# Kernel tuning notes

Hardware: AMD Instinct MI355X
Metric: run time of the kernel (lower is better)

Reference implementation:

```python
import jax, jax.numpy as jnp
import numpy as np

B, N, M = 4096, 512, 64
SEQ_W = 8
HID, CTRL_OUT = 256, 128
SHIFT_VEC = (-1, 0, 1)
L = len(SHIFT_VEC)
PARAM_SIZE = M + 1 + 1 + L + 1  # k(M), beta, g, s(L), gamma
# circular-shift gather indices: idx[i, j] = (i + shift_vec[j]) mod N
IDX = np.mod(np.arange(N)[:, None] + np.array(SHIFT_VEC)[None, :], N)


def setup_inputs() -> dict:
    key = jax.random.key(0)
    ks = jax.random.split(key, 12)
    def w(k, shape, fan_in):
        return jax.random.normal(k, shape, jnp.float32) / np.sqrt(fan_in).astype(np.float32)
    in_size = SEQ_W + 1 + M  # controller input: x (seq_width+1) + prev_read (M)
    wr = jax.random.uniform(ks[3], (B, N), jnp.float32)
    wr = wr / wr.sum(axis=1, keepdims=True)
    ww = jax.random.uniform(ks[4], (B, N), jnp.float32)
    ww = ww / ww.sum(axis=1, keepdims=True)
    return {
        "x": jax.random.normal(ks[0], (B, SEQ_W + 1), jnp.float32),
        "prev_read": jax.random.normal(ks[1], (B, M), jnp.float32),
        "bank": jax.random.uniform(ks[2], (B, N, M), jnp.float32) * 0.1 + 1e-6,
        "w_read": wr,
        "w_write": ww,
        "ctrl_W0": w(ks[5], (in_size, HID), in_size), "ctrl_b0": jnp.zeros(HID, jnp.float32),
        "ctrl_W1": w(ks[6], (HID, HID), HID), "ctrl_b1": jnp.zeros(HID, jnp.float32),
        "ctrl_Wout": w(ks[7], (HID, CTRL_OUT), HID), "ctrl_bout": jnp.zeros(CTRL_OUT, jnp.float32),
        "repr_W": w(ks[8], (CTRL_OUT, 2 * PARAM_SIZE + 2 * M), CTRL_OUT),
        "repr_b": jnp.zeros(2 * PARAM_SIZE + 2 * M, jnp.float32),
        "out_W": w(ks[9], (CTRL_OUT + M, SEQ_W), CTRL_OUT + M),
        "out_b": jnp.zeros(SEQ_W, jnp.float32),
    }


def _split(v):
    # k [B,M], beta [B,1], g [B,1], s [B,L], gamma [B,1]
    return v[:, :M], v[:, M:M + 1], v[:, M + 1:M + 2], v[:, M + 2:M + 2 + L], v[:, -1:]


def _address(param, w_prev, bank):
    k, beta, g, s, gamma = param
    kt = jnp.tanh(k)
    # cosine similarity along M (torch CosineSimilarity, eps=1e-8)
    dot = jnp.einsum('bnm,bm->bn', bank, kt)
    denom = jnp.linalg.norm(bank, axis=2) * jnp.linalg.norm(kt, axis=1, keepdims=True)
    cos = dot / jnp.maximum(denom, 1e-8)
    wc = jax.nn.softmax(jax.nn.softplus(beta) * cos, axis=1)
    gg = jax.nn.sigmoid(g)
    wg = gg * wc + (1.0 - gg) * w_prev
    sm = jax.nn.softmax(s, axis=1)
    # vectorized circular shift: ws[b,i] = sum_j wg[b,(i+shift_j)%N] * sm[b,j]
    ws = jnp.einsum('bnl,bl->bn', wg[:, IDX], sm)
    gamma = jax.nn.softplus(gamma) + 1.0
    wsh = ws ** gamma
    return wsh / wsh.sum(axis=1, keepdims=True)


def reference(x, prev_read, bank, w_read, w_write,
              ctrl_W0, ctrl_b0, ctrl_W1, ctrl_b1, ctrl_Wout, ctrl_bout,
              repr_W, repr_b, out_W, out_b):
    ctrl_in = jnp.concatenate([x, prev_read], axis=1)
    h = jax.nn.leaky_relu(ctrl_in @ ctrl_W0 + ctrl_b0)
    h = jax.nn.leaky_relu(h @ ctrl_W1 + ctrl_b1)
    ctrl_out = jnp.tanh(h @ ctrl_Wout + ctrl_bout)
    reprx = ctrl_out @ repr_W + repr_b
    read_param = _split(reprx[:, :PARAM_SIZE])
    write_param = _split(reprx[:, PARAM_SIZE:2 * PARAM_SIZE])
    e = jax.nn.sigmoid(reprx[:, 2 * PARAM_SIZE:2 * PARAM_SIZE + M])
    a = jnp.tanh(reprx[:, 2 * PARAM_SIZE + M:])
    rw = _address(read_param, w_read, bank)
    read = jnp.einsum('bn,bnm->bm', rw, bank)  # memory read
    wwt = _address(write_param, w_write, bank)
    # erase then add: bank - w*e + w*a
    new_bank = bank + wwt[:, :, None] * (a - e)[:, None, :]
    seq_out = jax.nn.sigmoid(jnp.concatenate([ctrl_out, read], axis=1) @ out_W + out_b)
    return seq_out, new_bank
```

## Files before the change

kernel.cpp:

```cpp
#include <hip/hip_runtime.h>
#include <hip/hip_bf16.h>
#include <math.h>

#define B_TOT 4096
#define NN 512
#define MM 64
#define HID 256
#define COUT 128
#define PSZ 70
#define REPRN 268
#define IN_SZ 73
#define WS_STRIDE 352
#define BT 8


__device__ __forceinline__ float sigmoidf_(float v){ return 1.f/(1.f+expf(-v)); }
__device__ __forceinline__ float softplusf_(float v){ return v > 20.f ? v : log1pf(expf(v)); }
__device__ __forceinline__ float leakyf_(float v){ return v >= 0.f ? v : 0.01f*v; }

__device__ __forceinline__ float wave_sum(float v){
  #pragma unroll
  for (int o = 32; o; o >>= 1) v += __shfl_xor(v, o);
  return v;
}
__device__ __forceinline__ float wave_max(float v){
  #pragma unroll
  for (int o = 32; o; o >>= 1) v = fmaxf(v, __shfl_xor(v, o));
  return v;
}
__device__ float block_sum(float v, float* red){
  v = wave_sum(v);
  int w = threadIdx.x >> 6, l = threadIdx.x & 63;
  __syncthreads();
  if (l == 0) red[w] = v;
  __syncthreads();
  return red[0] + red[1] + red[2] + red[3];
}
__device__ float block_max(float v, float* red){
  v = wave_max(v);
  int w = threadIdx.x >> 6, l = threadIdx.x & 63;
  __syncthreads();
  if (l == 0) red[w] = v;
  __syncthreads();
  return fmaxf(fmaxf(red[0], red[1]), fmaxf(red[2], red[3]));
}

__global__ __launch_bounds__(256) void k_ctrl(
    const float* __restrict__ x, const float* __restrict__ prev_read,
    const float* __restrict__ W0, const float* __restrict__ b0,
    const float* __restrict__ W1, const float* __restrict__ b1,
    const float* __restrict__ Wout, const float* __restrict__ bout,
    const float* __restrict__ rW, const float* __restrict__ rb,
    float* __restrict__ pws)
{
  __shared__ float cin[BT][80];
  __shared__ float sA[BT][256];
  __shared__ float sB[BT][256];
  __shared__ float sR[BT][272];
  const int t = threadIdx.x;
  const int bbase = blockIdx.x * BT;

  for (int idx = t; idx < BT * IN_SZ; idx += 256){
    int bb = idx / IN_SZ, i = idx - bb * IN_SZ;
    int b = bbase + bb;
    cin[bb][i] = (i < 9) ? x[b * 9 + i] : prev_read[b * MM + (i - 9)];
  }
  __syncthreads();

  {
    float acc[BT];
    #pragma unroll
    for (int bb = 0; bb < BT; ++bb) acc[bb] = 0.f;
    for (int i = 0; i < IN_SZ; ++i){
      float w = W0[i * 256 + t];
      #pragma unroll
      for (int bb = 0; bb < BT; ++bb) acc[bb] += cin[bb][i] * w;
    }
    float bias = b0[t];
    #pragma unroll
    for (int bb = 0; bb < BT; ++bb) sA[bb][t] = leakyf_(acc[bb] + bias);
  }
  __syncthreads();

  {
    float acc[BT];
    #pragma unroll
    for (int bb = 0; bb < BT; ++bb) acc[bb] = 0.f;
    for (int i = 0; i < 256; ++i){
      float w = W1[i * 256 + t];
      #pragma unroll
      for (int bb = 0; bb < BT; ++bb) acc[bb] += sA[bb][i] * w;
    }
    float bias = b1[t];
    #pragma unroll
    for (int bb = 0; bb < BT; ++bb) sB[bb][t] = leakyf_(acc[bb] + bias);
  }
  __syncthreads();

  if (t < COUT){
    float acc[BT];
    #pragma unroll
    for (int bb = 0; bb < BT; ++bb) acc[bb] = 0.f;
    for (int i = 0; i < 256; ++i){
      float w = Wout[i * COUT + t];
      #pragma unroll
      for (int bb = 0; bb < BT; ++bb) acc[bb] += sB[bb][i] * w;
    }
    float bias = bout[t];
    #pragma unroll
    for (int bb = 0; bb < BT; ++bb){
      float v = tanhf(acc[bb] + bias);
      sA[bb][t] = v;
      pws[(size_t)(bbase + bb) * WS_STRIDE + t] = v;
    }
  }
  __syncthreads();

  {
    float acc1[BT], acc2[BT];
    #pragma unroll
    for (int bb = 0; bb < BT; ++bb){ acc1[bb] = 0.f; acc2[bb] = 0.f; }
    const bool has2 = (t + 256) < REPRN;
    for (int i = 0; i < COUT; ++i){
      float w1 = rW[i * REPRN + t];
      float w2 = has2 ? rW[i * REPRN + t + 256] : 0.f;
      #pragma unroll
      for (int bb = 0; bb < BT; ++bb){
        float c = sA[bb][i];
        acc1[bb] += c * w1;
        acc2[bb] += c * w2;
      }
    }
    float r1 = rb[t];
    float r2 = has2 ? rb[t + 256] : 0.f;
    #pragma unroll
    for (int bb = 0; bb < BT; ++bb){
      sR[bb][t] = acc1[bb] + r1;
      if (has2) sR[bb][t + 256] = acc2[bb] + r2;
    }
  }
  __syncthreads();

  for (int bb = 0; bb < BT; ++bb){
    float* pb = pws + (size_t)(bbase + bb) * WS_STRIDE;
    if (t < 64){
      float kt = tanhf(sR[bb][t]);
      pb[128 + t] = kt;
      float s = wave_sum(kt * kt);
      if (t == 0) pb[320] = sqrtf(s);
    } else if (t < 128){
      int m = t - 64;
      float kt = tanhf(sR[bb][PSZ + m]);
      pb[192 + m] = kt;
      float s = wave_sum(kt * kt);
      if (m == 0) pb[328] = sqrtf(s);
    } else if (t < 192){
      int m = t - 128;
      float e = sigmoidf_(sR[bb][2 * PSZ + m]);
      float a = tanhf(sR[bb][2 * PSZ + MM + m]);
      pb[256 + m] = a - e;
    } else if (t == 192 || t == 193){
      int off = (t == 192) ? 0 : PSZ;
      int po  = (t == 192) ? 320 : 328;
      float beta = sR[bb][off + 64];
      float g    = sR[bb][off + 65];
      float s0 = sR[bb][off + 66], s1 = sR[bb][off + 67], s2 = sR[bb][off + 68];
      float gm = sR[bb][off + 69];
      pb[po + 1] = softplusf_(beta);
      pb[po + 2] = sigmoidf_(g);
      float mx = fmaxf(s0, fmaxf(s1, s2));
      float e0 = expf(s0 - mx), e1 = expf(s1 - mx), e2 = expf(s2 - mx);
      float inv = 1.f / (e0 + e1 + e2);
      pb[po + 3] = e0 * inv; pb[po + 4] = e1 * inv; pb[po + 5] = e2 * inv;
      pb[po + 6] = softplusf_(gm) + 1.f;
    }
  }
}

__device__ void address_head(const float* __restrict__ dot, const float* __restrict__ ssv,
                             float knorm, float beta, float g,
                             float sm0, float sm1, float sm2, float gamma,
                             const float* __restrict__ wprev,
                             float* tmp, float* wfin, float* red)
{
  const int t = threadIdx.x;
  float c1 = dot[t]       / fmaxf(sqrtf(ssv[t])       * knorm, 1e-8f);
  float c2 = dot[t + 256] / fmaxf(sqrtf(ssv[t + 256]) * knorm, 1e-8f);
  float v1 = beta * c1, v2 = beta * c2;
  float vmax = block_max(fmaxf(v1, v2), red);
  float e1 = expf(v1 - vmax), e2 = expf(v2 - vmax);
  float S = block_sum(e1 + e2, red);
  float inv = 1.f / S;
  float wg1 = g * (e1 * inv) + (1.f - g) * wprev[t];
  float wg2 = g * (e2 * inv) + (1.f - g) * wprev[t + 256];
  tmp[t] = wg1; tmp[t + 256] = wg2;
  __syncthreads();
  float ws1 = tmp[(t + 511) & 511] * sm0 + wg1 * sm1 + tmp[(t + 1) & 511] * sm2;
  float ws2 = tmp[(t + 255) & 511] * sm0 + wg2 * sm1 + tmp[(t + 257) & 511] * sm2;
  float p1 = powf(ws1, gamma), p2 = powf(ws2, gamma);
  float S2 = block_sum(p1 + p2, red);
  float inv2 = 1.f / S2;
  wfin[t] = p1 * inv2; wfin[t + 256] = p2 * inv2;
  __syncthreads();
}

__global__ __launch_bounds__(256) void k_head(
    const float* __restrict__ bank,
    const float* __restrict__ w_read, const float* __restrict__ w_write,
    const float* __restrict__ outW, const float* __restrict__ outb,
    const float* __restrict__ pws,
    float* __restrict__ out)
{
  __shared__ float dotr[512], dotw[512], ssv[512], tmp[512], wfr[512], wfw[512];
  __shared__ float red[4];
  __shared__ float readpart[4][64];
  __shared__ float readv[64];

  const int b = blockIdx.x;
  const int t = threadIdx.x;
  const int lane = t & 63, wave = t >> 6;
  const int mg = lane & 15;
  const int rsub = lane >> 4;

  const float* bankB = bank + (size_t)b * (NN * MM);
  const float* pb = pws + (size_t)b * WS_STRIDE;

  const float4 ktr = *(const float4*)(pb + 128 + mg * 4);
  const float4 ktw = *(const float4*)(pb + 192 + mg * 4);

  for (int it = 0; it < 32; ++it){
    int n = it * 16 + wave * 4 + rsub;
    float4 p = *(const float4*)(bankB + n * MM + mg * 4);
    float dr = p.x * ktr.x + p.y * ktr.y + p.z * ktr.z + p.w * ktr.w;
    float dw = p.x * ktw.x + p.y * ktw.y + p.z * ktw.z + p.w * ktw.w;
    float sq = p.x * p.x + p.y * p.y + p.z * p.z + p.w * p.w;
    #pragma unroll
    for (int msk = 1; msk < 16; msk <<= 1){
      dr += __shfl_xor(dr, msk);
      dw += __shfl_xor(dw, msk);
      sq += __shfl_xor(sq, msk);
    }
    if (mg == 0){ dotr[n] = dr; dotw[n] = dw; ssv[n] = sq; }
  }
  __syncthreads();

  address_head(dotr, ssv, pb[320], pb[321], pb[322], pb[323], pb[324], pb[325], pb[326],
               w_read + (size_t)b * NN, tmp, wfr, red);
  address_head(dotw, ssv, pb[328], pb[329], pb[330], pb[331], pb[332], pb[333], pb[334],
               w_write + (size_t)b * NN, tmp, wfw, red);

  const float4 ae4 = *(const float4*)(pb + 256 + mg * 4);
  float* outBank = out + (size_t)B_TOT * 8 + (size_t)b * (NN * MM);
  float4 racc = make_float4(0.f, 0.f, 0.f, 0.f);
  for (int it = 0; it < 32; ++it){
    int n = it * 16 + wave * 4 + rsub;
    float4 p = *(const float4*)(bankB + n * MM + mg * 4);
    float wr = wfr[n], wwn = wfw[n];
    float4 q;
    q.x = p.x + wwn * ae4.x; q.y = p.y + wwn * ae4.y;
    q.z = p.z + wwn * ae4.z; q.w = p.w + wwn * ae4.w;
    *(float4*)(outBank + n * MM + mg * 4) = q;
    racc.x += wr * p.x; racc.y += wr * p.y; racc.z += wr * p.z; racc.w += wr * p.w;
  }
  racc.x += __shfl_xor(racc.x, 16); racc.x += __shfl_xor(racc.x, 32);
  racc.y += __shfl_xor(racc.y, 16); racc.y += __shfl_xor(racc.y, 32);
  racc.z += __shfl_xor(racc.z, 16); racc.z += __shfl_xor(racc.z, 32);
  racc.w += __shfl_xor(racc.w, 16); racc.w += __shfl_xor(racc.w, 32);
  if (lane < 16){
    readpart[wave][mg * 4 + 0] = racc.x;
    readpart[wave][mg * 4 + 1] = racc.y;
    readpart[wave][mg * 4 + 2] = racc.z;
    readpart[wave][mg * 4 + 3] = racc.w;
  }
  __syncthreads();
  if (t < 64) readv[t] = readpart[0][t] + readpart[1][t] + readpart[2][t] + readpart[3][t];
  __syncthreads();

  if (t < 8){
    float acc = outb[t];
    for (int i = 0; i < COUT; ++i) acc += pb[i] * outW[i * 8 + t];
    for (int m = 0; m < MM; ++m)   acc += readv[m] * outW[(COUT + m) * 8 + t];
    out[(size_t)b * 8 + t] = sigmoidf_(acc);
  }
}

extern "C" void kernel_launch(void* const* d_in, const int* in_sizes, int n_in,
                              void* d_out, int out_size, void* d_ws, size_t ws_size,
                              hipStream_t stream) {
  const float* x         = (const float*)d_in[0];
  const float* prev_read = (const float*)d_in[1];
  const float* bank      = (const float*)d_in[2];
  const float* w_read    = (const float*)d_in[3];
  const float* w_write   = (const float*)d_in[4];
  const float* W0        = (const float*)d_in[5];
  const float* b0        = (const float*)d_in[6];
  const float* W1        = (const float*)d_in[7];
  const float* b1        = (const float*)d_in[8];
  const float* Wout      = (const float*)d_in[9];
  const float* bout      = (const float*)d_in[10];
  const float* rW        = (const float*)d_in[11];
  const float* rb        = (const float*)d_in[12];
  const float* outW      = (const float*)d_in[13];
  const float* outb      = (const float*)d_in[14];
  float* out = (float*)d_out;
  float* pws = (float*)d_ws;

  k_ctrl<<<dim3(B_TOT / BT), dim3(256), 0, stream>>>(
      x, prev_read, W0, b0, W1, b1, Wout, bout, rW, rb, pws);
  k_head<<<dim3(B_TOT), dim3(256), 0, stream>>>(
      bank, w_read, w_write, outW, outb, pws, out);
}
```

Baseline: 1.067 ms.

## Cache each batch's bank slice in registers and widen head kernel to 512 threads

The head kernel now runs 512 threads per batch row and loads that row's bank slice once into registers (16 float4 per thread). The second pass, which writes the updated bank and accumulates the read vector, reuses those registers instead of reading the bank from global memory again, so bank reads are halved. The addressing and reductions are reworked for 8 waves, and the final output projection is spread over 64 threads with shuffle reductions. The cost is high register pressure (64 floats of bank per thread under launch_bounds(512,2)), which could spill or cut occupancy.

```diff
diff --git a/kernel.cpp b/kernel.cpp
--- a/kernel.cpp
+++ b/kernel.cpp
@@ -28,21 +28,28 @@
   for (int o = 32; o; o >>= 1) v = fmaxf(v, __shfl_xor(v, o));
   return v;
 }
-__device__ float block_sum(float v, float* red){
+
+__device__ float block_sum8(float v, float* red){
   v = wave_sum(v);
   int w = threadIdx.x >> 6, l = threadIdx.x & 63;
   __syncthreads();
   if (l == 0) red[w] = v;
   __syncthreads();
-  return red[0] + red[1] + red[2] + red[3];
-}
-__device__ float block_max(float v, float* red){
+  float s = 0.f;
+  #pragma unroll
+  for (int i = 0; i < 8; ++i) s += red[i];
+  return s;
+}
+__device__ float block_max8(float v, float* red){
   v = wave_max(v);
   int w = threadIdx.x >> 6, l = threadIdx.x & 63;
   __syncthreads();
   if (l == 0) red[w] = v;
   __syncthreads();
-  return fmaxf(fmaxf(red[0], red[1]), fmaxf(red[2], red[3]));
+  float m = red[0];
+  #pragma unroll
+  for (int i = 1; i < 8; ++i) m = fmaxf(m, red[i]);
+  return m;
 }
 
 __global__ __launch_bounds__(256) void k_ctrl(
@@ -184,27 +191,22 @@
                              float* tmp, float* wfin, float* red)
 {
   const int t = threadIdx.x;
-  float c1 = dot[t]       / fmaxf(sqrtf(ssv[t])       * knorm, 1e-8f);
-  float c2 = dot[t + 256] / fmaxf(sqrtf(ssv[t + 256]) * knorm, 1e-8f);
-  float v1 = beta * c1, v2 = beta * c2;
-  float vmax = block_max(fmaxf(v1, v2), red);
-  float e1 = expf(v1 - vmax), e2 = expf(v2 - vmax);
-  float S = block_sum(e1 + e2, red);
-  float inv = 1.f / S;
-  float wg1 = g * (e1 * inv) + (1.f - g) * wprev[t];
-  float wg2 = g * (e2 * inv) + (1.f - g) * wprev[t + 256];
-  tmp[t] = wg1; tmp[t + 256] = wg2;
-  __syncthreads();
-  float ws1 = tmp[(t + 511) & 511] * sm0 + wg1 * sm1 + tmp[(t + 1) & 511] * sm2;
-  float ws2 = tmp[(t + 255) & 511] * sm0 + wg2 * sm1 + tmp[(t + 257) & 511] * sm2;
-  float p1 = powf(ws1, gamma), p2 = powf(ws2, gamma);
-  float S2 = block_sum(p1 + p2, red);
-  float inv2 = 1.f / S2;
-  wfin[t] = p1 * inv2; wfin[t + 256] = p2 * inv2;
-  __syncthreads();
-}
-
-__global__ __launch_bounds__(256) void k_head(
+  float c = dot[t] / fmaxf(sqrtf(ssv[t]) * knorm, 1e-8f);
+  float v = beta * c;
+  float vmax = block_max8(v, red);
+  float e = expf(v - vmax);
+  float S = block_sum8(e, red);
+  float wg = g * (e / S) + (1.f - g) * wprev[t];
+  tmp[t] = wg;
+  __syncthreads();
+  float ws = tmp[(t + 511) & 511] * sm0 + wg * sm1 + tmp[(t + 1) & 511] * sm2;
+  float p = powf(ws, gamma);
+  float S2 = block_sum8(p, red);
+  wfin[t] = p / S2;
+  __syncthreads();
+}
+
+__global__ __launch_bounds__(512, 2) void k_head(
     const float* __restrict__ bank,
     const float* __restrict__ w_read, const float* __restrict__ w_write,
     const float* __restrict__ outW, const float* __restrict__ outb,
@@ -212,8 +214,8 @@
     float* __restrict__ out)
 {
   __shared__ float dotr[512], dotw[512], ssv[512], tmp[512], wfr[512], wfw[512];
-  __shared__ float red[4];
-  __shared__ float readpart[4][64];
+  __shared__ float red[8];
+  __shared__ float readpart[8][64];
   __shared__ float readv[64];
 
   const int b = blockIdx.x;
@@ -228,9 +230,16 @@
   const float4 ktr = *(const float4*)(pb + 128 + mg * 4);
   const float4 ktw = *(const float4*)(pb + 192 + mg * 4);
 
-  for (int it = 0; it < 32; ++it){
-    int n = it * 16 + wave * 4 + rsub;
-    float4 p = *(const float4*)(bankB + n * MM + mg * 4);
+  float4 bank_r[16];
+  #pragma unroll
+  for (int it = 0; it < 16; ++it){
+    int n = it * 32 + wave * 4 + rsub;
+    bank_r[it] = *(const float4*)(bankB + n * MM + mg * 4);
+  }
+
+  #pragma unroll
+  for (int it = 0; it < 16; ++it){
+    float4 p = bank_r[it];
     float dr = p.x * ktr.x + p.y * ktr.y + p.z * ktr.z + p.w * ktr.w;
     float dw = p.x * ktw.x + p.y * ktw.y + p.z * ktw.z + p.w * ktw.w;
     float sq = p.x * p.x + p.y * p.y + p.z * p.z + p.w * p.w;
@@ -240,7 +249,10 @@
       dw += __shfl_xor(dw, msk);
       sq += __shfl_xor(sq, msk);
     }
-    if (mg == 0){ dotr[n] = dr; dotw[n] = dw; ssv[n] = sq; }
+    if (mg == 0){
+      int n = it * 32 + wave * 4 + rsub;
+      dotr[n] = dr; dotw[n] = dw; ssv[n] = sq;
+    }
   }
   __syncthreads();
 
@@ -252,9 +264,10 @@
   const float4 ae4 = *(const float4*)(pb + 256 + mg * 4);
   float* outBank = out + (size_t)B_TOT * 8 + (size_t)b * (NN * MM);
   float4 racc = make_float4(0.f, 0.f, 0.f, 0.f);
-  for (int it = 0; it < 32; ++it){
-    int n = it * 16 + wave * 4 + rsub;
-    float4 p = *(const float4*)(bankB + n * MM + mg * 4);
+  #pragma unroll
+  for (int it = 0; it < 16; ++it){
+    int n = it * 32 + wave * 4 + rsub;
+    float4 p = bank_r[it];
     float wr = wfr[n], wwn = wfw[n];
     float4 q;
     q.x = p.x + wwn * ae4.x; q.y = p.y + wwn * ae4.y;
@@ -273,14 +286,23 @@
     readpart[wave][mg * 4 + 3] = racc.w;
   }
   __syncthreads();
-  if (t < 64) readv[t] = readpart[0][t] + readpart[1][t] + readpart[2][t] + readpart[3][t];
-  __syncthreads();
-
-  if (t < 8){
-    float acc = outb[t];
-    for (int i = 0; i < COUT; ++i) acc += pb[i] * outW[i * 8 + t];
-    for (int m = 0; m < MM; ++m)   acc += readv[m] * outW[(COUT + m) * 8 + t];
-    out[(size_t)b * 8 + t] = sigmoidf_(acc);
+  if (t < 64){
+    float s = 0.f;
+    #pragma unroll
+    for (int w = 0; w < 8; ++w) s += readpart[w][t];
+    readv[t] = s;
+  }
+  __syncthreads();
+
+  if (t < 64){
+    int j = t >> 3, s = t & 7;
+    float acc = 0.f;
+    for (int i = s; i < COUT; i += 8) acc += pb[i] * outW[i * 8 + j];
+    for (int m = s; m < MM; m += 8)   acc += readv[m] * outW[(COUT + m) * 8 + j];
+    acc += __shfl_xor(acc, 1);
+    acc += __shfl_xor(acc, 2);
+    acc += __shfl_xor(acc, 4);
+    if (s == 0) out[(size_t)b * 8 + j] = sigmoidf_(acc + outb[j]);
   }
 }
 
@@ -307,6 +329,6 @@
 
   k_ctrl<<<dim3(B_TOT / BT), dim3(256), 0, stream>>>(
       x, prev_read, W0, b0, W1, b1, Wout, bout, rW, rb, pws);
-  k_head<<<dim3(B_TOT), dim3(256), 0, stream>>>(
+  k_head<<<dim3(B_TOT), dim3(512), 0, stream>>>(
       bank, w_read, w_write, outW, outb, pws, out);
 }
```

After: 1.040 ms. -2.5%, faster.
